# Optimization experiments

Measured on AMD Instinct MI355X. Metric: run time of the kernel, lower is better.

Reference implementation:

```python
import jax, jax.numpy as jnp
import numpy as np

B, C, H, L = 4, 1, 1024, 8192
KD, NS = 64, 4  # kernel_dim, num_scales


def _interp_linear(x, out_len):
    """F.interpolate(mode='linear', align_corners=False) along last axis."""
    in_len = x.shape[-1]
    if out_len == in_len:
        return x
    scale = out_len / in_len
    coord = (jnp.arange(out_len, dtype=jnp.float32) + 0.5) / scale - 0.5
    coord = jnp.clip(coord, 0.0, in_len - 1)
    lo = jnp.floor(coord).astype(jnp.int32)
    hi = jnp.minimum(lo + 1, in_len - 1)
    w = coord - lo.astype(jnp.float32)
    return x[..., lo] * (1.0 - w) + x[..., hi] * w


def setup_inputs() -> dict:
    key = jax.random.key(0)
    ks = jax.random.split(key, 8)
    u = jax.random.normal(ks[0], (B, H, L), jnp.float32)
    k0 = jax.random.normal(ks[1], (C, H, KD), jnp.float32)
    k1 = jax.random.normal(ks[2], (C, H, KD), jnp.float32)
    k2 = jax.random.normal(ks[3], (C, H, KD), jnp.float32)
    k3 = jax.random.normal(ks[4], (C, H, KD), jnp.float32)
    D = jax.random.normal(ks[5], (C, H), jnp.float32)
    W = jax.random.normal(ks[6], (H, C * H), jnp.float32) / np.float32(np.sqrt(C * H))
    b = jnp.zeros((H,), jnp.float32)
    return {"u": u, "k0": k0, "k1": k1, "k2": k2, "k3": k3, "D": D, "W": W, "b": b}


def reference(u, k0, k1, k2, k3, D, W, b):
    Lq = u.shape[-1]
    kernels = [k0, k1, k2, k3]
    total = KD * 2 ** (NS - 1)  # 512
    # multi-scale kernel build: interpolate -> right-pad -> scale -> sum
    parts = []
    for i in range(NS):
        ki = _interp_linear(kernels[i], KD * 2 ** i)
        ki = jnp.pad(ki, ((0, 0), (0, 0), (0, total - KD * 2 ** i)))
        parts.append(ki * (2.0 ** (NS - i - 1)))
    k = parts[0] + parts[1] + parts[2] + parts[3]  # (C,H,512)
    # fit to sequence length L
    if k.shape[-1] > Lq:
        k = k[..., :Lq]
    elif k.shape[-1] < Lq:
        k = jnp.pad(k, ((0, 0), (0, 0), (0, Lq - k.shape[-1])))
    # detached kernel norm
    knorm = jax.lax.stop_gradient(
        jnp.linalg.norm(k, axis=-1, keepdims=True))
    k = k / knorm
    # FFT long convolution
    n = 2 * Lq
    k_f = jnp.fft.rfft(k, n=n)              # (C,H,L+1) complex
    u_f = jnp.fft.rfft(u, n=n)              # (B,H,L+1) complex
    y_f = jnp.einsum('bhl,chl->bchl', u_f, k_f)
    y = jnp.fft.irfft(y_f, n=n)[..., :Lq]   # (B,C,H,L)
    # D skip (outer product)
    y = y + jnp.einsum('bhl,ch->bchl', u, D)
    y = y.reshape(y.shape[0], C * H, Lq)    # (B,C*H,L)
    # activation (exact gelu, torch default), dropout=Identity, norm=Identity
    y = jax.nn.gelu(y, approximate=False)
    # output_linear: 1x1 conv (C*H -> H) with bias, Identity post-activation
    y = jnp.einsum('bfl,of->bol', y, W) + b[None, :, None]
    return y
```

## Files before the change

### kernel.cpp

```cpp
#include <hip/hip_runtime.h>
#include <cstdint>
#include <cstddef>

#define HH 1024
#define LL 8192
#define NB 4
#define KD 64
#define KLEN 512

typedef float v4f  __attribute__((ext_vector_type(4)));
typedef float v16f __attribute__((ext_vector_type(16)));
typedef short v8s  __attribute__((ext_vector_type(8)));

__device__ __forceinline__ unsigned short f2bf(float f) {
  union { float f; unsigned int u; } x; x.f = f;
  unsigned int r = x.u + 0x7fffu + ((x.u >> 16) & 1u);
  return (unsigned short)(r >> 16);
}

__global__ __launch_bounds__(512) void build_k_kernel(
    const float* __restrict__ k0, const float* __restrict__ k1,
    const float* __restrict__ k2, const float* __restrict__ k3,
    float* __restrict__ kout) {
  __shared__ float lk[4][KD];
  __shared__ float red[512];
  const int h = blockIdx.x;
  const int t = threadIdx.x;
  if (t < 256) {
    int i = t >> 6, j = t & 63;
    const float* src = (i == 0) ? k0 : (i == 1) ? k1 : (i == 2) ? k2 : k3;
    lk[i][j] = src[h * KD + j];
  }
  __syncthreads();
  float kt = 0.f;
#pragma unroll
  for (int i = 0; i < 4; i++) {
    int len = KD << i;
    if (t < len) {
      float inv = 1.0f / (float)(1 << i);
      float c = ((float)t + 0.5f) * inv - 0.5f;
      c = fminf(fmaxf(c, 0.0f), 63.0f);
      int lo = (int)floorf(c);
      int hi = min(lo + 1, 63);
      float w = c - (float)lo;
      float v = lk[i][lo] * (1.0f - w) + lk[i][hi] * w;
      kt += v * (float)(1 << (3 - i));
    }
  }
  red[t] = kt * kt;
  __syncthreads();
  for (int s = 256; s > 0; s >>= 1) {
    if (t < s) red[t] += red[t + s];
    __syncthreads();
  }
  float norm = sqrtf(red[0]);
  kout[h * KLEN + t] = kt / norm;
}

__global__ void w2bf_kernel(const float* __restrict__ W,
                            unsigned short* __restrict__ Wb, int n) {
  int i = blockIdx.x * blockDim.x + threadIdx.x;
  if (i < n) Wb[i] = f2bf(W[i]);
}

__global__ __launch_bounds__(256) void conv_kernel(
    const float* __restrict__ u, const float* __restrict__ kk,
    const float* __restrict__ D, unsigned short* __restrict__ g) {
  __shared__ __align__(16) unsigned short Apk[34 * 512];
  __shared__ __align__(16) unsigned short su[512 + LL];
  __shared__ __align__(16) float skk[KLEN];

  const int h = blockIdx.x;
  const int tid = threadIdx.x;
  const int w = tid >> 6;
  const int ln = tid & 63;
  const int n = ln & 31;
  const int q = ln >> 5;

  if (tid < 128) *(float4*)(skk + tid * 4) = *(const float4*)(kk + (size_t)h * KLEN + tid * 4);
  __syncthreads();

#pragma unroll 4
  for (int e = 0; e < 68; ++e) {
    int idx = e * 256 + tid;
    int s = idx >> 9;
    int lane = (idx >> 3) & 63;
    int j = idx & 7;
    int m = lane & 31, q2 = lane >> 5;
    int c = ((s & 1) << 4) + (q2 << 3) + j;
    int t = ((s >> 1) << 5) + m - c;
    Apk[idx] = (t >= 0 && t < KLEN) ? f2bf(skk[t]) : (unsigned short)0;
  }

  const float Dh = D[h];
  const int b_base0 = 512 + 32 * (w * 64 + n) + 8 * q;
  const int b_base1 = b_base0 + 1024;

  for (int b = 0; b < NB; ++b) {
    __syncthreads();
    const float* __restrict__ urow = u + ((size_t)b * HH + h) * LL;
    if (tid < 64) {
      uint4 z; z.x = 0; z.y = 0; z.z = 0; z.w = 0;
      *(uint4*)(su + tid * 8) = z;
    }
#pragma unroll
    for (int r = 0; r < 8; ++r) {
      int i = r * 1024 + tid * 4;
      float4 v = *(const float4*)(urow + i);
      uint2 p;
      p.x = (unsigned)f2bf(v.x) | ((unsigned)f2bf(v.y) << 16);
      p.y = (unsigned)f2bf(v.z) | ((unsigned)f2bf(v.w) << 16);
      *(uint2*)(su + 512 + i) = p;
    }
    __syncthreads();

    v16f acc0, acc1;
#pragma unroll
    for (int r = 0; r < 16; ++r) { acc0[r] = 0.f; acc1[r] = 0.f; }

#pragma unroll
    for (int s = 0; s < 34; ++s) {
      const int off = ((s & 1) << 4) - ((s >> 1) << 5);
      v8s af = *(const v8s*)(Apk + (s << 9) + (ln << 3));
      v8s b0 = *(const v8s*)(su + b_base0 + off);
      v8s b1 = *(const v8s*)(su + b_base1 + off);
      acc0 = __builtin_amdgcn_mfma_f32_32x32x16_bf16(af, b0, acc0, 0, 0, 0);
      acc1 = __builtin_amdgcn_mfma_f32_32x32x16_bf16(af, b1, acc1, 0, 0, 0);
    }

    unsigned short* grow = g + ((size_t)b * HH + h) * LL;
#pragma unroll
    for (int t = 0; t < 2; ++t) {
      const int i0 = w * 64 + t * 32;
#pragma unroll
      for (int rg = 0; rg < 4; ++rg) {
        const int l = 32 * (i0 + n) + 8 * rg + 4 * q;
        float4 uu = *(const float4*)(urow + l);
        const float* up = (const float*)&uu;
        unsigned short hb[4];
#pragma unroll
        for (int rr = 0; rr < 4; ++rr) {
          float y = (t ? acc1[rg * 4 + rr] : acc0[rg * 4 + rr]) + Dh * up[rr];
          float ge = 0.5f * y * (1.0f + erff(y * 0.70710678118654752f));
          hb[rr] = f2bf(ge);
        }
        uint2 p;
        p.x = (unsigned)hb[0] | ((unsigned)hb[1] << 16);
        p.y = (unsigned)hb[2] | ((unsigned)hb[3] << 16);
        *(uint2*)(grow + l) = p;
      }
    }
  }
}

__device__ __forceinline__ void gll16(const void* g, void* l) {
  __builtin_amdgcn_global_load_lds(
      (const __attribute__((address_space(1))) unsigned int*)g,
      (__attribute__((address_space(3))) unsigned int*)l, 16, 0, 0);
}

__global__ __launch_bounds__(256) void gemm_kernel(
    const unsigned short* __restrict__ A,
    const unsigned short* __restrict__ G,
    const float* __restrict__ bias, float* __restrict__ out) {
  __shared__ __align__(16) unsigned short sA[128 * 32];
  __shared__ __align__(16) unsigned int   sB[16 * 128];
  const int tid = threadIdx.x;
  const int wv = tid >> 6, ln = tid & 63;

  const int bid0 = blockIdx.x;
  const int swz = (bid0 & 7) * 256 + (bid0 >> 3);
  const int mt = swz & 7, nt = swz >> 3;
  const int o0 = mt * 128;
  const int bb = nt >> 6;
  const int l0 = (nt & 63) * 128;
  const int m16 = ln & 15, q4 = ln >> 4;
  const int wm = wv & 1, wn = wv >> 1;

  v4f acc[4][4];
#pragma unroll
  for (int i = 0; i < 4; i++)
#pragma unroll
    for (int j = 0; j < 4; j++) {
      v4f z = {0.f, 0.f, 0.f, 0.f};
      acc[i][j] = z;
    }

  const unsigned short* gptrA[4];
  unsigned short* lptrA[4];
  if (wv < 2) {
#pragma unroll
    for (int qq = 0; qq < 4; qq++) {
      int c = wv * 4 + qq;
      int rr = c * 16 + (ln >> 2);
      int cc = (ln & 3) * 8;
      gptrA[qq] = A + (size_t)(o0 + rr) * HH + cc;
      lptrA[qq] = sA + c * 512;
    }
  }

  const int kp = tid >> 4;
  const int seg = tid & 15;
  char* sBb = (char*)sB;
  const unsigned xw = ((unsigned)(kp & 1) << 4) | ((unsigned)((kp >> 2) & 1) << 6);
  const unsigned wb0 = (unsigned)(kp * 512 + seg * 32);
  const unsigned short* gB0 = G + ((size_t)bb * HH + kp * 2) * LL + l0 + seg * 8;
  const unsigned short* gB1 = gB0 + LL;

  const int nloc = wn * 64 + m16;

  uint4 ra = *(const uint4*)(gB0);
  uint4 rb = *(const uint4*)(gB1);

  for (int kk = 0; kk < 32; kk++) {
    union { uint4 u; unsigned short s[8]; } ua, ub;
    ua.u = ra; ub.u = rb;
    unsigned pk[8];
#pragma unroll
    for (int i = 0; i < 8; ++i)
      pk[i] = (unsigned)ua.s[i] | ((unsigned)ub.s[i] << 16);
    *(uint4*)(sBb + ((wb0)      ^ xw)) = *(const uint4*)&pk[0];
    *(uint4*)(sBb + ((wb0 + 16) ^ xw)) = *(const uint4*)&pk[4];

    if (wv < 2) {
#pragma unroll
      for (int qq = 0; qq < 4; qq++) gll16(gptrA[qq] + kk * 32, lptrA[qq]);
    }
    __syncthreads();

    if (kk < 31) {
      ra = *(const uint4*)(gB0 + (size_t)(kk + 1) * 32 * LL);
      rb = *(const uint4*)(gB1 + (size_t)(kk + 1) * 32 * LL);
    }

    v8s af[4];
#pragma unroll
    for (int i = 0; i < 4; i++)
      af[i] = *(const v8s*)&sA[(wm * 64 + i * 16 + m16) * 32 + q4 * 8];
    v8s bf4[4];
#pragma unroll
    for (int j = 0; j < 4; j++) {
      union { v8s v; unsigned w[4]; } u;
#pragma unroll
      for (int p = 0; p < 4; p++) {
        unsigned boff = ((unsigned)((q4 * 4 + p) * 128 + nloc + j * 16) << 2)
                        ^ ((unsigned)(p & 1) << 4) ^ ((unsigned)(q4 & 1) << 6);
        u.w[p] = *(const unsigned*)(sBb + boff);
      }
      bf4[j] = u.v;
    }
#pragma unroll
    for (int i = 0; i < 4; i++)
#pragma unroll
      for (int j = 0; j < 4; j++)
        acc[i][j] = __builtin_amdgcn_mfma_f32_16x16x32_bf16(af[i], bf4[j], acc[i][j], 0, 0, 0);
    __syncthreads();
  }

#pragma unroll
  for (int i = 0; i < 4; i++) {
    const int ob = o0 + wm * 64 + i * 16 + q4 * 4;
#pragma unroll
    for (int j = 0; j < 4; j++) {
      const int l = l0 + wn * 64 + j * 16 + m16;
#pragma unroll
      for (int r = 0; r < 4; r++) {
        const int o = ob + r;
        out[((size_t)bb * HH + o) * LL + l] = acc[i][j][r] + bias[o];
      }
    }
  }
}

extern "C" void kernel_launch(void* const* d_in, const int* in_sizes, int n_in,
                              void* d_out, int out_size, void* d_ws, size_t ws_size,
                              hipStream_t stream) {
  const float* u   = (const float*)d_in[0];
  const float* k0  = (const float*)d_in[1];
  const float* k1  = (const float*)d_in[2];
  const float* k2  = (const float*)d_in[3];
  const float* k3  = (const float*)d_in[4];
  const float* D   = (const float*)d_in[5];
  const float* W   = (const float*)d_in[6];
  const float* bia = (const float*)d_in[7];
  float* out = (float*)d_out;

  char* ws = (char*)d_ws;
  unsigned short* g  = (unsigned short*)ws;
  float* kws         = (float*)(ws + (size_t)67108864);
  unsigned short* Wb = (unsigned short*)(ws + (size_t)69206016);

  build_k_kernel<<<HH, 512, 0, stream>>>(k0, k1, k2, k3, kws);
  w2bf_kernel<<<(HH * HH + 255) / 256, 256, 0, stream>>>(W, Wb, HH * HH);
  conv_kernel<<<HH, 256, 0, stream>>>(u, kws, D, g);
  gemm_kernel<<<8 * 256, 256, 0, stream>>>(Wb, g, bia, out);
}
```

Measured before the change: 399.2 us.

## Double-buffer GEMM LDS with swizzled layouts and prefetch; swizzle conv LDS input

The GEMM kernel now uses double-buffered A and B tiles in LDS. Global loads for B are prefetched two iterations ahead, and waits use explicit waitcnt plus a single barrier per step. The A and B LDS layouts are XOR-swizzled so each fragment loads as one 16-byte read, and MFMA issue is wrapped in setprio to overlap memory with compute. The conv kernel's shared u buffer also gets an XOR swizzle to reduce bank conflicts. The cost is more LDS, more hand-written wait counts that must stay correct, and higher register pressure.

```diff
diff --git a/kernel.cpp b/kernel.cpp
--- a/kernel.cpp
+++ b/kernel.cpp
@@ -63,6 +63,8 @@
   if (i < n) Wb[i] = f2bf(W[i]);
 }
 
+__device__ __forceinline__ int suswz(int b) { return b ^ (((b >> 7) & 3) << 4); }
+
 __global__ __launch_bounds__(256) void conv_kernel(
     const float* __restrict__ u, const float* __restrict__ kk,
     const float* __restrict__ D, unsigned short* __restrict__ g) {
@@ -76,6 +78,7 @@
   const int ln = tid & 63;
   const int n = ln & 31;
   const int q = ln >> 5;
+  char* sub = (char*)su;
 
   if (tid < 128) *(float4*)(skk + tid * 4) = *(const float4*)(kk + (size_t)h * KLEN + tid * 4);
   __syncthreads();
@@ -93,15 +96,15 @@
   }
 
   const float Dh = D[h];
-  const int b_base0 = 512 + 32 * (w * 64 + n) + 8 * q;
-  const int b_base1 = b_base0 + 1024;
+  const int bbyte0 = 1024 + 64 * (w * 64 + n) + 16 * q;
+  const int bbyte1 = bbyte0 + 2048;
 
   for (int b = 0; b < NB; ++b) {
     __syncthreads();
     const float* __restrict__ urow = u + ((size_t)b * HH + h) * LL;
     if (tid < 64) {
       uint4 z; z.x = 0; z.y = 0; z.z = 0; z.w = 0;
-      *(uint4*)(su + tid * 8) = z;
+      *(uint4*)(sub + suswz(tid * 16)) = z;
     }
 #pragma unroll
     for (int r = 0; r < 8; ++r) {
@@ -110,7 +113,7 @@
       uint2 p;
       p.x = (unsigned)f2bf(v.x) | ((unsigned)f2bf(v.y) << 16);
       p.y = (unsigned)f2bf(v.z) | ((unsigned)f2bf(v.w) << 16);
-      *(uint2*)(su + 512 + i) = p;
+      *(uint2*)(sub + suswz(1024 + 2 * i)) = p;
     }
     __syncthreads();
 
@@ -120,10 +123,10 @@
 
 #pragma unroll
     for (int s = 0; s < 34; ++s) {
-      const int off = ((s & 1) << 4) - ((s >> 1) << 5);
+      const int offb = ((s & 1) << 5) - ((s >> 1) << 6);
       v8s af = *(const v8s*)(Apk + (s << 9) + (ln << 3));
-      v8s b0 = *(const v8s*)(su + b_base0 + off);
-      v8s b1 = *(const v8s*)(su + b_base1 + off);
+      v8s b0 = *(const v8s*)(sub + suswz(bbyte0 + offb));
+      v8s b1 = *(const v8s*)(sub + suswz(bbyte1 + offb));
       acc0 = __builtin_amdgcn_mfma_f32_32x32x16_bf16(af, b0, acc0, 0, 0, 0);
       acc1 = __builtin_amdgcn_mfma_f32_32x32x16_bf16(af, b1, acc1, 0, 0, 0);
     }
@@ -163,8 +166,8 @@
     const unsigned short* __restrict__ A,
     const unsigned short* __restrict__ G,
     const float* __restrict__ bias, float* __restrict__ out) {
-  __shared__ __align__(16) unsigned short sA[128 * 32];
-  __shared__ __align__(16) unsigned int   sB[16 * 128];
+  __shared__ __align__(16) unsigned short sA[2][4096];
+  __shared__ __align__(16) unsigned int   sB[2][2048];
   const int tid = threadIdx.x;
   const int wv = tid >> 6, ln = tid & 63;
 
@@ -186,75 +189,137 @@
       acc[i][j] = z;
     }
 
-  const unsigned short* gptrA[4];
-  unsigned short* lptrA[4];
-  if (wv < 2) {
-#pragma unroll
-    for (int qq = 0; qq < 4; qq++) {
-      int c = wv * 4 + qq;
-      int rr = c * 16 + (ln >> 2);
-      int cc = (ln & 3) * 8;
-      gptrA[qq] = A + (size_t)(o0 + rr) * HH + cc;
-      lptrA[qq] = sA + c * 512;
-    }
-  }
-
-  const int kp = tid >> 4;
-  const int seg = tid & 15;
-  char* sBb = (char*)sB;
-  const unsigned xw = ((unsigned)(kp & 1) << 4) | ((unsigned)((kp >> 2) & 1) << 6);
-  const unsigned wb0 = (unsigned)(kp * 512 + seg * 32);
-  const unsigned short* gB0 = G + ((size_t)bb * HH + kp * 2) * LL + l0 + seg * 8;
+  const unsigned short* gA[2];
+  int lA[2];
+  {
+    const int cc = (((ln & 3) ^ ((ln >> 3) & 3)) << 3);
+#pragma unroll
+    for (int qq = 0; qq < 2; qq++) {
+      const int c = wv * 2 + qq;
+      const int rr = c * 16 + (ln >> 2);
+      gA[qq] = A + (size_t)(o0 + rr) * HH + cc;
+      lA[qq] = c * 512;
+    }
+  }
+
+  const int pr = tid >> 4, seg = tid & 15;
+  const unsigned short* gB0 = G + ((size_t)bb * HH + 2 * pr) * LL + l0 + seg * 8;
   const unsigned short* gB1 = gB0 + LL;
-
-  const int nloc = wn * 64 + m16;
-
-  uint4 ra = *(const uint4*)(gB0);
-  uint4 rb = *(const uint4*)(gB1);
-
-  for (int kk = 0; kk < 32; kk++) {
-    union { uint4 u; unsigned short s[8]; } ua, ub;
-    ua.u = ra; ub.u = rb;
-    unsigned pk[8];
-#pragma unroll
-    for (int i = 0; i < 8; ++i)
-      pk[i] = (unsigned)ua.s[i] | ((unsigned)ub.s[i] << 16);
-    *(uint4*)(sBb + ((wb0)      ^ xw)) = *(const uint4*)&pk[0];
-    *(uint4*)(sBb + ((wb0 + 16) ^ xw)) = *(const uint4*)&pk[4];
-
-    if (wv < 2) {
-#pragma unroll
-      for (int qq = 0; qq < 4; qq++) gll16(gptrA[qq] + kk * 32, lptrA[qq]);
-    }
-    __syncthreads();
-
-    if (kk < 31) {
-      ra = *(const uint4*)(gB0 + (size_t)(kk + 1) * 32 * LL);
-      rb = *(const uint4*)(gB1 + (size_t)(kk + 1) * 32 * LL);
-    }
-
-    v8s af[4];
-#pragma unroll
-    for (int i = 0; i < 4; i++)
-      af[i] = *(const v8s*)&sA[(wm * 64 + i * 16 + m16) * 32 + q4 * 8];
-    v8s bf4[4];
-#pragma unroll
-    for (int j = 0; j < 4; j++) {
-      union { v8s v; unsigned w[4]; } u;
-#pragma unroll
-      for (int p = 0; p < 4; p++) {
-        unsigned boff = ((unsigned)((q4 * 4 + p) * 128 + nloc + j * 16) << 2)
-                        ^ ((unsigned)(p & 1) << 4) ^ ((unsigned)(q4 & 1) << 6);
-        u.w[p] = *(const unsigned*)(sBb + boff);
-      }
-      bf4[j] = u.v;
-    }
+  int wby[8];
+#pragma unroll
+  for (int e = 0; e < 8; e++) {
+    int l = seg * 8 + e;
+    int byi = (pr >> 2) * 2048 + l * 16 + (pr & 3) * 4;
+    wby[e] = byi ^ (((l >> 3) & 7) << 4);
+  }
+
+  int aby[4], bby[4];
+#pragma unroll
+  for (int i = 0; i < 4; i++) {
+    int row = wm * 64 + i * 16 + m16;
+    aby[i] = (row * 64 + q4 * 16) ^ (((m16 >> 1) & 3) << 4);
+  }
+#pragma unroll
+  for (int j = 0; j < 4; j++) {
+    int l = wn * 64 + j * 16 + m16;
+    bby[j] = (q4 * 2048 + l * 16) ^ (((l >> 3) & 7) << 4);
+  }
+
+  auto stageA = [&](int buf, int kbase) {
+#pragma unroll
+    for (int qq = 0; qq < 2; qq++) gll16(gA[qq] + kbase, &sA[buf][lA[qq]]);
+  };
+  auto packB = [&](int buf, const uint4& r0, const uint4& r1) {
+    union { uint4 u; unsigned short s[8]; } ua, ub; ua.u = r0; ub.u = r1;
+    char* base = (char*)sB[buf];
+#pragma unroll
+    for (int e = 0; e < 8; e++) {
+      unsigned v = (unsigned)ua.s[e] | ((unsigned)ub.s[e] << 16);
+      *(unsigned*)(base + wby[e]) = v;
+    }
+  };
+
+  uint4 p0, p1, c0, c1;
+  stageA(0, 0);
+  __builtin_amdgcn_sched_barrier(0);
+  p0 = *(const uint4*)(gB0); p1 = *(const uint4*)(gB1);
+  __builtin_amdgcn_sched_barrier(0);
+  c0 = *(const uint4*)(gB0 + (size_t)32 * LL);
+  c1 = *(const uint4*)(gB1 + (size_t)32 * LL);
+  __builtin_amdgcn_sched_barrier(0);
+  packB(0, p0, p1);
+  asm volatile("s_waitcnt vmcnt(2) lgkmcnt(0)" ::: "memory");
+  __builtin_amdgcn_s_barrier();
+
+  for (int kk = 0; kk < 30; ++kk) {
+    const int p = kk & 1;
+    v8s af[4], bf4[4];
+    const char* ab = (const char*)sA[p];
+    const char* bbc = (const char*)sB[p];
+#pragma unroll
+    for (int i = 0; i < 4; i++) af[i] = *(const v8s*)(ab + aby[i]);
+#pragma unroll
+    for (int j = 0; j < 4; j++) bf4[j] = *(const v8s*)(bbc + bby[j]);
+    stageA(p ^ 1, (kk + 1) * 32);
+    __builtin_amdgcn_sched_barrier(0);
+    uint4 n0 = *(const uint4*)(gB0 + (size_t)(kk + 2) * 32 * LL);
+    uint4 n1 = *(const uint4*)(gB1 + (size_t)(kk + 2) * 32 * LL);
+    asm volatile("s_waitcnt lgkmcnt(0)" ::: "memory");
+    __builtin_amdgcn_sched_barrier(0);
+    __builtin_amdgcn_s_setprio(1);
 #pragma unroll
     for (int i = 0; i < 4; i++)
 #pragma unroll
       for (int j = 0; j < 4; j++)
         acc[i][j] = __builtin_amdgcn_mfma_f32_16x16x32_bf16(af[i], bf4[j], acc[i][j], 0, 0, 0);
-    __syncthreads();
+    __builtin_amdgcn_s_setprio(0);
+    asm volatile("s_waitcnt vmcnt(4)" ::: "memory");
+    packB(p ^ 1, c0, c1);
+    c0 = n0; c1 = n1;
+    asm volatile("s_waitcnt vmcnt(2) lgkmcnt(0)" ::: "memory");
+    __builtin_amdgcn_s_barrier();
+  }
+
+  {
+    v8s af[4], bf4[4];
+    const char* ab = (const char*)sA[0];
+    const char* bbc = (const char*)sB[0];
+#pragma unroll
+    for (int i = 0; i < 4; i++) af[i] = *(const v8s*)(ab + aby[i]);
+#pragma unroll
+    for (int j = 0; j < 4; j++) bf4[j] = *(const v8s*)(bbc + bby[j]);
+    stageA(1, 31 * 32);
+    asm volatile("s_waitcnt lgkmcnt(0)" ::: "memory");
+    __builtin_amdgcn_sched_barrier(0);
+    __builtin_amdgcn_s_setprio(1);
+#pragma unroll
+    for (int i = 0; i < 4; i++)
+#pragma unroll
+      for (int j = 0; j < 4; j++)
+        acc[i][j] = __builtin_amdgcn_mfma_f32_16x16x32_bf16(af[i], bf4[j], acc[i][j], 0, 0, 0);
+    __builtin_amdgcn_s_setprio(0);
+    asm volatile("s_waitcnt vmcnt(2)" ::: "memory");
+    packB(1, c0, c1);
+    asm volatile("s_waitcnt vmcnt(0) lgkmcnt(0)" ::: "memory");
+    __builtin_amdgcn_s_barrier();
+  }
+  {
+    v8s af[4], bf4[4];
+    const char* ab = (const char*)sA[1];
+    const char* bbc = (const char*)sB[1];
+#pragma unroll
+    for (int i = 0; i < 4; i++) af[i] = *(const v8s*)(ab + aby[i]);
+#pragma unroll
+    for (int j = 0; j < 4; j++) bf4[j] = *(const v8s*)(bbc + bby[j]);
+    asm volatile("s_waitcnt lgkmcnt(0)" ::: "memory");
+    __builtin_amdgcn_sched_barrier(0);
+    __builtin_amdgcn_s_setprio(1);
+#pragma unroll
+    for (int i = 0; i < 4; i++)
+#pragma unroll
+      for (int j = 0; j < 4; j++)
+        acc[i][j] = __builtin_amdgcn_mfma_f32_16x16x32_bf16(af[i], bf4[j], acc[i][j], 0, 0, 0);
+    __builtin_amdgcn_s_setprio(0);
   }
 
 #pragma unroll
```

New measurement: 406.7 us. About the same (+1.9%).
